# Optimization experiments

Measured on AMD Instinct MI355X. Metric: run time of the kernel, lower is better.

Reference implementation:

```python
import jax, jax.numpy as jnp
import numpy as np

NUM_TOKENS = 32000
DIM = 1024
DEPTH = 4
HEADS = 16
DIM_HEAD = 64
FF_MULT = 4
DH_FF = int(DIM * FF_MULT * 2 / 3)  # 2730
B, N = 2, 2048
ROPE_THETA = 10000.0


def setup_inputs() -> dict:
    key = jax.random.key(0)
    ks = jax.random.split(key, 8)
    s = 0.02
    return {
        "tokens": jax.random.randint(ks[0], (B, N), 0, NUM_TOKENS),
        "token_emb": jax.random.normal(ks[1], (NUM_TOKENS, DIM)) * s,
        "attn_norm_w": jnp.ones((DEPTH, DIM)),
        "wqkv": jax.random.normal(ks[2], (DEPTH, DIM, 3 * HEADS * DIM_HEAD)) * s,
        "wo": jax.random.normal(ks[3], (DEPTH, HEADS * DIM_HEAD, DIM)) * s,
        "ff_norm_w": jnp.ones((DEPTH, DIM)),
        "ff_w1": jax.random.normal(ks[4], (DEPTH, DIM, 2 * DH_FF)) * s,
        "ff_b1": jnp.zeros((DEPTH, 2 * DH_FF)),
        "ff_w2": jax.random.normal(ks[5], (DEPTH, DH_FF, DIM)) * s,
        "ff_b2": jnp.zeros((DEPTH, DIM)),
        "final_norm_w": jnp.ones((DIM,)),
        "logits_w": jax.random.normal(ks[6], (DIM, NUM_TOKENS)) * s,
        "logits_b": jnp.zeros((NUM_TOKENS,)),
    }


def rmsnorm(x, w):
    eps = jnp.finfo(x.dtype).eps  # torch RMSNorm default eps
    var = jnp.mean(jnp.square(x), axis=-1, keepdims=True)
    return x * jax.lax.rsqrt(var + eps) * w


def rotate_half(x):
    x1, x2 = jnp.split(x, 2, axis=-1)
    return jnp.concatenate((-x2, x1), axis=-1)


def apply_rope(pos, t):
    return t * jnp.cos(pos) + rotate_half(t) * jnp.sin(pos)


def reference(tokens, token_emb, attn_norm_w, wqkv, wo, ff_norm_w,
              ff_w1, ff_b1, ff_w2, ff_b2, final_norm_w, logits_w, logits_b):
    b, n = tokens.shape
    x = token_emb[tokens]  # [b, n, dim]

    # rotary embedding table [n, dim_head]
    inv_freq = ROPE_THETA ** (-(jnp.arange(0, DIM_HEAD, 2, dtype=jnp.float32) / DIM_HEAD))
    freqs = jnp.arange(n, dtype=jnp.float32)[:, None] * inv_freq[None, :]
    pos = jnp.concatenate((freqs, freqs), axis=-1)

    scale = DIM_HEAD ** -0.5
    causal = jnp.triu(jnp.ones((n, n), dtype=bool), 1)

    for l in range(DEPTH):
        # --- attention ---
        h = rmsnorm(x, attn_norm_w[l])
        qkv = jnp.einsum('bnd,de->bne', h, wqkv[l])
        qkv = qkv.reshape(b, n, 3, HEADS, DIM_HEAD)
        qkv = jnp.transpose(qkv, (2, 0, 3, 1, 4))  # [3, b, h, n, d]
        q, k, v = qkv[0], qkv[1], qkv[2]
        q = apply_rope(pos, q)
        k = apply_rope(pos, k)
        q = q * scale
        sim = jnp.einsum('bhid,bhjd->bhij', q, k)
        sim = jnp.where(causal, -jnp.finfo(sim.dtype).max, sim)
        attn = jax.nn.softmax(sim, axis=-1)
        out = jnp.einsum('bhij,bhjd->bhid', attn, v)
        out = jnp.transpose(out, (0, 2, 1, 3)).reshape(b, n, HEADS * DIM_HEAD)
        x = jnp.einsum('bne,ed->bnd', out, wo[l]) + x

        # --- GEGLU feedforward ---
        h = rmsnorm(x, ff_norm_w[l])
        u = jnp.einsum('bnd,de->bne', h, ff_w1[l]) + ff_b1[l]
        u1, gate = jnp.split(u, 2, axis=-1)
        g = jax.nn.gelu(gate, approximate=False) * u1
        x = jnp.einsum('bne,ed->bnd', g, ff_w2[l]) + ff_b2[l] + x

    embed = rmsnorm(x, final_norm_w)
    logits = jnp.einsum('bnd,dv->bnv', embed, logits_w) + logits_b
    return logits
```

## Files before the change

### kernel.cpp

```cpp
#include <hip/hip_runtime.h>
#include <math.h>
#include <stdint.h>


using short8v = __attribute__((ext_vector_type(8))) short;
using f32x4   = __attribute__((ext_vector_type(4))) float;

__device__ __forceinline__ float b2f(short s) {
    union { unsigned u; float f; } v; v.u = ((unsigned)(unsigned short)s) << 16; return v.f;
}
__device__ __forceinline__ short f2b(float f) {
    union { float f; unsigned u; } v; v.f = f;
    unsigned r = v.u + 0x7FFFu + ((v.u >> 16) & 1u);
    return (short)(r >> 16);
}

__device__ __forceinline__ void mfma_n(f32x4& d, short8v a, short8v b) {
    asm("v_mfma_f32_16x16x32_bf16 %0, %1, %2, %0" : "+v"(d) : "v"(a), "v"(b));
}
__device__ __forceinline__ void mfma_f(f32x4& d, short8v a, short8v b) {
    asm("s_nop 1\n\tv_mfma_f32_16x16x32_bf16 %0, %1, %2, %0" : "+v"(d) : "v"(a), "v"(b));
}
#define MFMA_FENCE() do { __builtin_amdgcn_sched_barrier(0); \
    asm volatile("s_nop 7\n\ts_nop 7"); \
    __builtin_amdgcn_sched_barrier(0); } while (0)

__device__ __forceinline__ void gload16(const void* g, void* l) {
    __builtin_amdgcn_global_load_lds(
        (const __attribute__((address_space(1))) unsigned int*)(uintptr_t)g,
        (__attribute__((address_space(3))) unsigned int*)(uintptr_t)l,
        16, 0, 0);
}

#define BARX() do { asm volatile("" ::: "memory"); \
    __builtin_amdgcn_s_barrier(); asm volatile("" ::: "memory"); } while (0)
#define VMN(n) asm volatile("s_waitcnt vmcnt(" #n ")" ::: "memory")
#define LGKM0() do { asm volatile("s_waitcnt lgkmcnt(0)" ::: "memory"); \
    __builtin_amdgcn_sched_barrier(0); } while (0)

__global__ void rope_table_k(float* __restrict__ ct, float* __restrict__ st) {
    int i = blockIdx.x * 256 + threadIdx.x;
    int n = i >> 5, j = i & 31;
    float freq = expf(-(float)j * (9.210340371976184f / 32.f));
    float a = (float)n * freq;
    ct[i] = cosf(a);
    st[i] = sinf(a);
}

__global__ void embed_k(const int* __restrict__ tok, const float* __restrict__ emb,
                        float* __restrict__ x) {
    int row = blockIdx.x;
    int tk = tok[row];
    const float4* src = (const float4*)(emb + (size_t)tk * 1024);
    float4* dst = (float4*)(x + (size_t)row * 1024);
    dst[threadIdx.x] = src[threadIdx.x];
}

__global__ void wconv_k(const float* __restrict__ W, short* __restrict__ T,
                        int K, int N, int Kpad,
                        size_t w_lstride, size_t t_lstride) {
    W += blockIdx.z * w_lstride;
    T += blockIdx.z * t_lstride;
    int n0 = blockIdx.x * 32, k0 = blockIdx.y * 32;
    __shared__ float tile[32][33];
    int t = threadIdx.x;
    int kk = t >> 3, ns = (t & 7) * 4;
    float4 v = make_float4(0.f, 0.f, 0.f, 0.f);
    int gk = k0 + kk;
    if (gk < K) {
        if (n0 + ns + 3 < N) {
            v = *(const float4*)(W + (size_t)gk * N + n0 + ns);
        } else {
            float tmp[4] = {0.f, 0.f, 0.f, 0.f};
            #pragma unroll
            for (int j = 0; j < 4; ++j)
                if (n0 + ns + j < N) tmp[j] = W[(size_t)gk * N + n0 + ns + j];
            v = make_float4(tmp[0], tmp[1], tmp[2], tmp[3]);
        }
    }
    tile[kk][ns + 0] = v.x; tile[kk][ns + 1] = v.y;
    tile[kk][ns + 2] = v.z; tile[kk][ns + 3] = v.w;
    __syncthreads();
    int nn = t >> 3, ks = (t & 7) * 4;
    short o[4];
    #pragma unroll
    for (int j = 0; j < 4; ++j) o[j] = f2b(tile[ks + j][nn]);
    *(int2*)(T + (size_t)(n0 + nn) * Kpad + k0 + ks) = *(int2*)o;
}

__global__ void rmsnorm_k(const float* __restrict__ x, const float* __restrict__ wt,
                          short* __restrict__ out) {
    int row = blockIdx.x;
    int t = threadIdx.x;
    const float* xr = x + (size_t)row * 1024;
    float4 v = ((const float4*)xr)[t];
    float ss = v.x * v.x + v.y * v.y + v.z * v.z + v.w * v.w;
    #pragma unroll
    for (int off = 32; off > 0; off >>= 1) ss += __shfl_down(ss, off, 64);
    __shared__ float red[4];
    if ((t & 63) == 0) red[t >> 6] = ss;
    __syncthreads();
    float tot = red[0] + red[1] + red[2] + red[3];
    float inv = rsqrtf(tot * (1.f / 1024.f) + 1.1920929e-7f);
    float4 wv = ((const float4*)wt)[t];
    int2 pk;
    pk.x = (int)(unsigned short)f2b(v.x * inv * wv.x) |
           ((int)(unsigned short)f2b(v.y * inv * wv.y) << 16);
    pk.y = (int)(unsigned short)f2b(v.z * inv * wv.z) |
           ((int)(unsigned short)f2b(v.w * inv * wv.w) << 16);
    *(int2*)(out + (size_t)row * 1024 + t * 4) = pk;
}

__global__ void rope_apply_k(short* __restrict__ qkv, const float* __restrict__ ct,
                             const float* __restrict__ st) {
    int gidx = blockIdx.x * 256 + threadIdx.x;
    int j  = gidx & 31;
    int r  = (gidx >> 5) & 4095;
    int hk = gidx >> 17;
    int qk = hk >> 4, h = hk & 15;
    int n = r & 2047;
    size_t base = (size_t)r * 3072 + (size_t)qk * 1024 + h * 64 + j;
    float a  = b2f(qkv[base]);
    float bv = b2f(qkv[base + 32]);
    float cc = ct[n * 32 + j], sv = st[n * 32 + j];
    float na = a * cc - bv * sv;
    float nb = bv * cc + a * sv;
    if (qk == 0) { na *= 0.125f; nb *= 0.125f; }
    qkv[base]      = f2b(na);
    qkv[base + 32] = f2b(nb);
}

__global__ void vt_k(const short* __restrict__ qkv, short* __restrict__ vt) {
    int id = blockIdx.x * 256 + threadIdx.x;
    int dt = id & 7, nt = (id >> 3) & 255, bh = id >> 11;
    int b = bh >> 4, h = bh & 15;
    short s[8][8];
    #pragma unroll
    for (int r = 0; r < 8; ++r)
        *(int4*)s[r] = *(const int4*)(qkv + (size_t)(b * 2048 + nt * 8 + r) * 3072
                                      + 2048 + h * 64 + dt * 8);
    #pragma unroll
    for (int cc = 0; cc < 8; ++cc) {
        short o4[8];
        #pragma unroll
        for (int r = 0; r < 8; ++r) o4[r] = s[r][cc];
        *(int4*)(vt + (size_t)(bh * 64 + dt * 8 + cc) * 2048 + nt * 8) = *(int4*)o4;
    }
}

__global__ void geglu_k(const short* __restrict__ u, short* __restrict__ gbuf) {
    int r = blockIdx.x;
    int c = blockIdx.y * 256 + threadIdx.x;
    if (c >= 2752) return;
    float v = 0.f;
    if (c < 2730) {
        float u1 = b2f(u[(size_t)r * 5460 + c]);
        float gt = b2f(u[(size_t)r * 5460 + 2730 + c]);
        v = 0.5f * gt * (1.f + erff(gt * 0.7071067811865475f)) * u1;
    }
    gbuf[(size_t)r * 2752 + c] = f2b(v);
}

template <bool BIAS, bool RES, bool OUTBF16>
__global__ __launch_bounds__(256, 2) void gemm2(
    const short* __restrict__ A, const short* __restrict__ Bt,
    const float* __restrict__ bias, const float* __restrict__ res,
    void* __restrict__ outp, int N, int lda, int ldb, int ksteps) {
    __shared__ __align__(16) short As[128 * 32];
    __shared__ __align__(16) short Bs[128 * 32];
    const int t = threadIdx.x;
    const int lane = t & 63;
    const int w = t >> 6, wm = w >> 1, wn = w & 1;
    const int c = lane & 15, g = lane >> 4;

    const int nwg = (int)gridDim.x;
    const int cpx = nwg >> 3;
    const int wg = ((int)blockIdx.x & 7) * cpx + ((int)blockIdx.x >> 3);
    const int m0 = (wg & 31) << 7;
    const int n0 = (wg >> 5) << 7;

    const int srow = w * 32 + (lane >> 2);
    const int sseg = (lane & 3) * 8;
    const short* ga0 = A  + (size_t)(m0 + srow) * lda + sseg;
    const short* ga1 = A  + (size_t)(m0 + srow + 16) * lda + sseg;
    const short* gb0 = Bt + (size_t)(n0 + srow) * ldb + sseg;
    const short* gb1 = Bt + (size_t)(n0 + srow + 16) * ldb + sseg;
    short* la0 = &As[(w * 2 + 0) * 512];
    short* la1 = &As[(w * 2 + 1) * 512];
    short* lb0 = &Bs[(w * 2 + 0) * 512];
    short* lb1 = &Bs[(w * 2 + 1) * 512];

    f32x4 acc[4][4] = {};

    for (int kt = 0; kt < ksteps; ++kt) {
        const int k0 = kt << 5;
        __syncthreads();
        gload16(ga0 + k0, la0);
        gload16(ga1 + k0, la1);
        gload16(gb0 + k0, lb0);
        gload16(gb1 + k0, lb1);
        __syncthreads();
        short8v af[4], bf[4];
        #pragma unroll
        for (int mi = 0; mi < 4; ++mi)
            af[mi] = *(const short8v*)&As[(wm * 64 + mi * 16 + c) * 32 + g * 8];
        #pragma unroll
        for (int ni = 0; ni < 4; ++ni)
            bf[ni] = *(const short8v*)&Bs[(wn * 64 + ni * 16 + c) * 32 + g * 8];
        #pragma unroll
        for (int mi = 0; mi < 4; ++mi)
            #pragma unroll
            for (int ni = 0; ni < 4; ++ni)
                mfma_n(acc[mi][ni], af[mi], bf[ni]);
    }
    MFMA_FENCE();
    #pragma unroll
    for (int mi = 0; mi < 4; ++mi) {
        #pragma unroll
        for (int ni = 0; ni < 4; ++ni) {
            int col = n0 + wn * 64 + ni * 16 + c;
            if (col < N) {
                float bv = BIAS ? bias[col] : 0.f;
                #pragma unroll
                for (int i = 0; i < 4; ++i) {
                    int row = m0 + wm * 64 + mi * 16 + g * 4 + i;
                    size_t off = (size_t)row * N + col;
                    float v = acc[mi][ni][i] + bv;
                    if (RES) v += res[off];
                    if (OUTBF16) ((short*)outp)[off] = f2b(v);
                    else         ((float*)outp)[off] = v;
                }
            }
        }
    }
}

template <bool BIAS, bool RES, bool OUTBF16>
__global__ __launch_bounds__(512, 1) void gemm3(
    const short* __restrict__ A, const short* __restrict__ Bt,
    const float* __restrict__ bias, const float* __restrict__ res,
    void* __restrict__ outp, int N, int lda, int ldb, int nrowsB, int KT) {
    __shared__ __align__(16) short L[49152];
    const int t = threadIdx.x;
    const int lane = t & 63;
    const int w = t >> 6;
    const int wm = w >> 2, wn = w & 3;
    const int c = lane & 15, g = lane >> 4;

    const int nwg = (int)gridDim.x, cpx = nwg >> 3;
    const int wg = ((int)blockIdx.x & 7) * cpx + ((int)blockIdx.x >> 3);
    const int m0 = (wg & 31) << 7;
    const int n0 = (wg >> 5) << 8;

    const int rS = t >> 3, sS = t & 7;
    const int sSw = (sS ^ (rS & 7)) << 3;
    size_t aoffh[2], broff[2][2];
    #pragma unroll
    for (int h = 0; h < 2; ++h)
        aoffh[h] = (size_t)(m0 + h * 64 + rS) * lda + sSw;
    #pragma unroll
    for (int h = 0; h < 2; ++h)
        #pragma unroll
        for (int i = 0; i < 2; ++i) {
            int brow = n0 + h * 128 + rS + i * 64;
            if (brow > nrowsB - 1) brow = nrowsB - 1;
            broff[h][i] = (size_t)brow * ldb + sSw;
        }
    short* ldsA[2][2];
    short* ldsB[2][2];
    #pragma unroll
    for (int p = 0; p < 2; ++p)
        #pragma unroll
        for (int h = 0; h < 2; ++h) {
            ldsA[p][h] = &L[(p * 2 + h) * 4096 + w * 512];
            ldsB[p][h] = &L[16384 + (p * 2 + h) * 8192 + w * 512];
        }

    const int cb0 = ((g * 8) ^ ((c & 7) * 8));
    const int vbA0 = wm * 4096 + c * 64 + cb0;
    const int vbA1 = vbA0 ^ 32;
    const int vbB0 = 16384 + (wn >> 1) * 8192 + (wn & 1) * 4096 + c * 64 + cb0;
    const int vbB1 = vbB0 ^ 32;

    #define STA3(p, h, kt) gload16(A + aoffh[h] + (kt) * 64, ldsA[p][h])
    #define STB3(p, h, kt) do { \
        gload16(Bt + broff[h][0] + (kt) * 64, ldsB[p][h]); \
        gload16(Bt + broff[h][1] + (kt) * 64, ldsB[p][h] + 4096); } while (0)
    #define LDA3(p, mi, ks) (*(const short8v*)&L[(p) * 8192 + (mi) * 1024 + ((ks) ? vbA1 : vbA0)])
    #define LDB3(p, ni, ks) (*(const short8v*)&L[(p) * 16384 + (ni) * 1024 + ((ks) ? vbB1 : vbB0)])
    #define MFMA8(MLO, NLO, BV) do { \
        _Pragma("unroll") for (int ks_ = 0; ks_ < 2; ++ks_) \
        _Pragma("unroll") for (int mi_ = 0; mi_ < 2; ++mi_) \
        _Pragma("unroll") for (int ni_ = 0; ni_ < 2; ++ni_) \
            mfma_n(acc[(MLO) + mi_][(NLO) + ni_], av[(MLO) + mi_][ks_], BV[(NLO) + ni_][ks_]); \
        } while (0)

    f32x4 acc[4][4] = {};
    short8v av[4][2], bc[4][2], bn[4][2];

    STB3(0, 1, 0); STB3(0, 0, 0); STA3(0, 0, 0); STA3(0, 1, 0);
    STB3(1, 1, 1); STB3(1, 0, 1); STA3(1, 0, 1); STA3(1, 1, 1);
    VMN(6);
    BARX();
    #pragma unroll
    for (int ni = 0; ni < 4; ++ni)
        #pragma unroll
        for (int ks = 0; ks < 2; ++ks)
            bc[ni][ks] = LDB3(0, ni, ks);
    LGKM0();
    BARX();
    asm volatile("s_nop 7\n\ts_nop 7");

    for (int KB = 0; KB < KT; KB += 2) {
        const bool st1 = (KB + 2 < KT);
        const bool st2 = (KB + 3 < KT);
        #pragma unroll
        for (int mi = 0; mi < 2; ++mi)
            #pragma unroll
            for (int ks = 0; ks < 2; ++ks) av[mi][ks] = LDA3(0, mi, ks);
        if (st1) STB3(0, 1, KB + 2);
        BARX();
        __builtin_amdgcn_s_setprio(1); MFMA8(0, 0, bc); __builtin_amdgcn_s_setprio(0);
        BARX();
        #pragma unroll
        for (int mi = 2; mi < 4; ++mi)
            #pragma unroll
            for (int ks = 0; ks < 2; ++ks) av[mi][ks] = LDA3(0, mi, ks);
        if (st1) { STB3(0, 0, KB + 2); VMN(6); } else { VMN(2); }
        BARX();
        __builtin_amdgcn_s_setprio(1); MFMA8(2, 0, bc); __builtin_amdgcn_s_setprio(0);
        BARX();
        #pragma unroll
        for (int ni = 0; ni < 2; ++ni)
            #pragma unroll
            for (int ks = 0; ks < 2; ++ks) bn[ni][ks] = LDB3(1, ni, ks);
        if (st1) STA3(0, 0, KB + 2);
        BARX();
        __builtin_amdgcn_s_setprio(1); MFMA8(0, 2, bc); __builtin_amdgcn_s_setprio(0);
        BARX();
        #pragma unroll
        for (int ni = 2; ni < 4; ++ni)
            #pragma unroll
            for (int ks = 0; ks < 2; ++ks) bn[ni][ks] = LDB3(1, ni, ks);
        if (st1) { STA3(0, 1, KB + 2); VMN(6); } else { VMN(0); }
        BARX();
        __builtin_amdgcn_s_setprio(1); MFMA8(2, 2, bc); __builtin_amdgcn_s_setprio(0);
        BARX();
        #pragma unroll
        for (int mi = 0; mi < 2; ++mi)
            #pragma unroll
            for (int ks = 0; ks < 2; ++ks) av[mi][ks] = LDA3(1, mi, ks);
        if (st2) STB3(1, 1, KB + 3);
        BARX();
        __builtin_amdgcn_s_setprio(1); MFMA8(0, 0, bn); __builtin_amdgcn_s_setprio(0);
        BARX();
        #pragma unroll
        for (int mi = 2; mi < 4; ++mi)
            #pragma unroll
            for (int ks = 0; ks < 2; ++ks) av[mi][ks] = LDA3(1, mi, ks);
        if (st2) STB3(1, 0, KB + 3);
        if (st1) VMN(6);
        BARX();
        __builtin_amdgcn_s_setprio(1); MFMA8(2, 0, bn); __builtin_amdgcn_s_setprio(0);
        BARX();
        if (st1) {
            #pragma unroll
            for (int ni = 0; ni < 2; ++ni)
                #pragma unroll
                for (int ks = 0; ks < 2; ++ks) bc[ni][ks] = LDB3(0, ni, ks);
        }
        if (st2) STA3(1, 0, KB + 3);
        BARX();
        __builtin_amdgcn_s_setprio(1); MFMA8(0, 2, bn); __builtin_amdgcn_s_setprio(0);
        BARX();
        if (st1) {
            #pragma unroll
            for (int ni = 2; ni < 4; ++ni)
                #pragma unroll
                for (int ks = 0; ks < 2; ++ks) bc[ni][ks] = LDB3(0, ni, ks);
        }
        if (st2) STA3(1, 1, KB + 3);
        if (st1) VMN(6);
        BARX();
        __builtin_amdgcn_s_setprio(1); MFMA8(2, 2, bn); __builtin_amdgcn_s_setprio(0);
        BARX();
    }

    MFMA_FENCE();
    #pragma unroll
    for (int mi = 0; mi < 4; ++mi) {
        #pragma unroll
        for (int ni = 0; ni < 4; ++ni) {
            int col = n0 + wn * 64 + ni * 16 + c;
            if (col < N) {
                float bv = BIAS ? bias[col] : 0.f;
                #pragma unroll
                for (int i = 0; i < 4; ++i) {
                    int row = m0 + wm * 64 + mi * 16 + g * 4 + i;
                    size_t off = (size_t)row * N + col;
                    float v = acc[mi][ni][i] + bv;
                    if (RES) v += res[off];
                    if (OUTBF16) ((short*)outp)[off] = f2b(v);
                    else         ((float*)outp)[off] = v;
                }
            }
        }
    }
    #undef STA3
    #undef STB3
    #undef LDA3
    #undef LDB3
    #undef MFMA8
}

__global__ __launch_bounds__(256, 2) void attn_fwd(
    const short* __restrict__ qkv, const short* __restrict__ vt,
    short* __restrict__ o) {
    const int qt = blockIdx.x, bh = blockIdx.y;
    const int b = bh >> 4, h = bh & 15;
    const int t = threadIdx.x, lane = t & 63, w = t >> 6;
    const int c = lane & 15, g = lane >> 4;
    __shared__ __align__(16) short Ks[128 * 72];
    __shared__ __align__(16) short Vs[64 * 136];
    __shared__ __align__(16) short Ps[128 * 136];

    #pragma unroll
    for (int i = 0; i < 4; ++i) {
        int idx = t + i * 256, r = idx >> 3, seg = idx & 7;
        *(int4*)&Ps[r * 136 + seg * 8] =
            *(const int4*)(qkv + (size_t)(b * 2048 + qt * 128 + r) * 3072 + h * 64 + seg * 8);
    }
    __syncthreads();
    short8v qf[2][2];
    #pragma unroll
    for (int mi = 0; mi < 2; ++mi)
        #pragma unroll
        for (int kk = 0; kk < 2; ++kk)
            qf[mi][kk] = *(const short8v*)&Ps[(w * 32 + mi * 16 + c) * 136 + kk * 32 + g * 8];

    f32x4 oacc[2][4] = {};
    float mrow[2][4], lrow[2][4];
    #pragma unroll
    for (int mi = 0; mi < 2; ++mi)
        #pragma unroll
        for (int i = 0; i < 4; ++i) { mrow[mi][i] = -3.0e38f; lrow[mi][i] = 0.f; }

    for (int jt = 0; jt <= qt; ++jt) {
        __syncthreads();
        #pragma unroll
        for (int i = 0; i < 4; ++i) {
            int idx = t + i * 256, r = idx >> 3, seg = idx & 7;
            *(int4*)&Ks[r * 72 + seg * 8] =
                *(const int4*)(qkv + (size_t)(b * 2048 + jt * 128 + r) * 3072
                               + 1024 + h * 64 + seg * 8);
        }
        #pragma unroll
        for (int i = 0; i < 4; ++i) {
            int idx = t + i * 256, d = idx >> 4, seg = idx & 15;
            *(int4*)&Vs[d * 136 + seg * 8] =
                *(const int4*)(vt + (size_t)(bh * 64 + d) * 2048 + jt * 128 + seg * 8);
        }
        __syncthreads();
        f32x4 sacc[2][8] = {};
        #pragma unroll
        for (int kk = 0; kk < 2; ++kk) {
            short8v kf[8];
            #pragma unroll
            for (int ni = 0; ni < 8; ++ni)
                kf[ni] = *(const short8v*)&Ks[(ni * 16 + c) * 72 + kk * 32 + g * 8];
            #pragma unroll
            for (int mi = 0; mi < 2; ++mi)
                #pragma unroll
                for (int ni = 0; ni < 8; ++ni) {
                    if (kk == 0) mfma_f(sacc[mi][ni], qf[mi][kk], kf[ni]);
                    else         mfma_n(sacc[mi][ni], qf[mi][kk], kf[ni]);
                }
        }
        MFMA_FENCE();
        if (jt == qt) {
            #pragma unroll
            for (int mi = 0; mi < 2; ++mi)
                #pragma unroll
                for (int ni = 0; ni < 8; ++ni)
                    #pragma unroll
                    for (int i = 0; i < 4; ++i) {
                        int qrow = w * 32 + mi * 16 + g * 4 + i;
                        int kcol = ni * 16 + c;
                        if (kcol > qrow) sacc[mi][ni][i] = -3.0e38f;
                    }
        }
        #pragma unroll
        for (int mi = 0; mi < 2; ++mi) {
            #pragma unroll
            for (int i = 0; i < 4; ++i) {
                float mx = sacc[mi][0][i];
                #pragma unroll
                for (int ni = 1; ni < 8; ++ni) mx = fmaxf(mx, sacc[mi][ni][i]);
                #pragma unroll
                for (int off = 1; off < 16; off <<= 1) mx = fmaxf(mx, __shfl_xor(mx, off, 64));
                float mnew = fmaxf(mrow[mi][i], mx);
                float alpha = __expf(mrow[mi][i] - mnew);
                mrow[mi][i] = mnew;
                float ls = 0.f;
                #pragma unroll
                for (int ni = 0; ni < 8; ++ni) {
                    float p = __expf(sacc[mi][ni][i] - mnew);
                    sacc[mi][ni][i] = p;
                    ls += p;
                }
                #pragma unroll
                for (int off = 1; off < 16; off <<= 1) ls += __shfl_xor(ls, off, 64);
                lrow[mi][i] = lrow[mi][i] * alpha + ls;
                #pragma unroll
                for (int df = 0; df < 4; ++df) oacc[mi][df][i] *= alpha;
            }
        }
        #pragma unroll
        for (int mi = 0; mi < 2; ++mi)
            #pragma unroll
            for (int ni = 0; ni < 8; ++ni)
                #pragma unroll
                for (int i = 0; i < 4; ++i)
                    Ps[(w * 32 + mi * 16 + g * 4 + i) * 136 + ni * 16 + c] =
                        f2b(sacc[mi][ni][i]);
        #pragma unroll
        for (int kk = 0; kk < 4; ++kk) {
            short8v pf[2], vf[4];
            #pragma unroll
            for (int mi = 0; mi < 2; ++mi)
                pf[mi] = *(const short8v*)&Ps[(w * 32 + mi * 16 + c) * 136 + kk * 32 + g * 8];
            #pragma unroll
            for (int df = 0; df < 4; ++df)
                vf[df] = *(const short8v*)&Vs[(df * 16 + c) * 136 + kk * 32 + g * 8];
            #pragma unroll
            for (int mi = 0; mi < 2; ++mi)
                #pragma unroll
                for (int df = 0; df < 4; ++df) {
                    if (kk == 0) mfma_f(oacc[mi][df], pf[mi], vf[df]);
                    else         mfma_n(oacc[mi][df], pf[mi], vf[df]);
                }
        }
    }
    MFMA_FENCE();
    #pragma unroll
    for (int mi = 0; mi < 2; ++mi)
        #pragma unroll
        for (int df = 0; df < 4; ++df)
            #pragma unroll
            for (int i = 0; i < 4; ++i) {
                int qrow = qt * 128 + w * 32 + mi * 16 + g * 4 + i;
                float v = oacc[mi][df][i] / lrow[mi][i];
                o[(size_t)(b * 2048 + qrow) * 1024 + h * 64 + df * 16 + c] = f2b(v);
            }
}

extern "C" void kernel_launch(void* const* d_in, const int* in_sizes, int n_in,
                              void* d_out, int out_size, void* d_ws, size_t ws_size,
                              hipStream_t stream) {
    (void)in_sizes; (void)n_in; (void)out_size; (void)ws_size;
    const int*   tokens = (const int*)d_in[0];
    const float* temb   = (const float*)d_in[1];
    const float* anw    = (const float*)d_in[2];
    const float* wqkv   = (const float*)d_in[3];
    const float* wo     = (const float*)d_in[4];
    const float* fnw    = (const float*)d_in[5];
    const float* fw1    = (const float*)d_in[6];
    const float* fb1    = (const float*)d_in[7];
    const float* fw2    = (const float*)d_in[8];
    const float* fb2    = (const float*)d_in[9];
    const float* finw   = (const float*)d_in[10];
    const float* lw     = (const float*)d_in[11];
    const float* lb     = (const float*)d_in[12];

    char* ws = (char*)d_ws;
    float* x    = (float*)(ws + 0);
    short* hb   = (short*)(ws + 16777216);
    short* qkv  = (short*)(ws + 25165824);
    short* ao   = (short*)(ws + 50331648);
    short* ub   = (short*)(ws + 58720256);
    short* gb   = (short*)(ws + 103448576);
    short* vtb  = (short*)(ws + 125992960);
    float* ct   = (float*)(ws + 134381568);
    float* st   = (float*)(ws + 134643712);
    short* qkvT = (short*)(ws + 134905856);
    short* woT  = (short*)(ws + 160071680);
    short* fw1T = (short*)(ws + 168460288);
    short* fw2T = (short*)(ws + 213549056);
    short* logT = (short*)(ws + 236093440);

    rope_table_k<<<256, 256, 0, stream>>>(ct, st);
    embed_k<<<4096, 256, 0, stream>>>(tokens, temb, x);

    wconv_k<<<dim3(96, 32, 4), 256, 0, stream>>>(
        wqkv, qkvT, 1024, 3072, 1024, (size_t)1024 * 3072, (size_t)3072 * 1024);
    wconv_k<<<dim3(32, 32, 4), 256, 0, stream>>>(
        wo, woT, 1024, 1024, 1024, (size_t)1024 * 1024, (size_t)1024 * 1024);
    wconv_k<<<dim3(172, 32, 4), 256, 0, stream>>>(
        fw1, fw1T, 1024, 5460, 1024, (size_t)1024 * 5460, (size_t)5504 * 1024);
    wconv_k<<<dim3(32, 86, 4), 256, 0, stream>>>(
        fw2, fw2T, 2730, 1024, 2752, (size_t)2730 * 1024, (size_t)1024 * 2752);
    wconv_k<<<dim3(1000, 32, 1), 256, 0, stream>>>(
        lw, logT, 1024, 32000, 1024, 0, 0);

    for (int l = 0; l < 4; ++l) {
        rmsnorm_k<<<4096, 256, 0, stream>>>(x, anw + l * 1024, hb);
        gemm3<false, false, true><<<32 * 12, 512, 0, stream>>>(
            hb, qkvT + (size_t)l * 3072 * 1024, nullptr, nullptr, qkv,
            3072, 1024, 1024, 3072, 16);
        rope_apply_k<<<16384, 256, 0, stream>>>(qkv, ct, st);
        vt_k<<<256, 256, 0, stream>>>(qkv, vtb);
        attn_fwd<<<dim3(16, 32), 256, 0, stream>>>(qkv, vtb, ao);
        gemm2<false, true, false><<<32 * 8, 256, 0, stream>>>(
            ao, woT + (size_t)l * 1024 * 1024, nullptr, x, x, 1024, 1024, 1024, 32);
        rmsnorm_k<<<4096, 256, 0, stream>>>(x, fnw + l * 1024, hb);
        gemm3<true, false, true><<<32 * 22, 512, 0, stream>>>(
            hb, fw1T + (size_t)l * 5504 * 1024, fb1 + l * 5460, nullptr, ub,
            5460, 1024, 1024, 5504, 16);
        geglu_k<<<dim3(4096, 11), 256, 0, stream>>>(ub, gb);
        gemm2<true, true, false><<<32 * 8, 256, 0, stream>>>(
            gb, fw2T + (size_t)l * 1024 * 2752, fb2 + l * 1024, x, x, 1024, 2752, 2752, 86);
    }
    rmsnorm_k<<<4096, 256, 0, stream>>>(x, finw, hb);
    gemm3<true, false, false><<<32 * 125, 512, 0, stream>>>(
        hb, logT, lb, nullptr, d_out, 32000, 1024, 1024, 32000, 16);
}
```

Baseline: 2.059 ms.

## Fuse RoPE into QKV GEMM epilogue and add larger-tile logits GEMM

Removes the separate rope_apply_k pass by applying rotary embedding and the q scale inside the QKV GEMM epilogue, where each wave's 64-column tile holds both halves of a head. Also adds a new gemm4 kernel with 256x256 tiles, two workgroups per CU and a different LDS staging layout, and uses it for the final 32000-wide logits projection. The fusion saves one read-modify-write pass over the qkv buffer per layer. The new logits kernel aims to raise operand reuse on the largest GEMM, at the cost of more accumulator registers and LDS per workgroup.

```diff
diff --git a/kernel.cpp b/kernel.cpp
--- a/kernel.cpp
+++ b/kernel.cpp
@@ -111,25 +111,6 @@
     *(int2*)(out + (size_t)row * 1024 + t * 4) = pk;
 }
 
-__global__ void rope_apply_k(short* __restrict__ qkv, const float* __restrict__ ct,
-                             const float* __restrict__ st) {
-    int gidx = blockIdx.x * 256 + threadIdx.x;
-    int j  = gidx & 31;
-    int r  = (gidx >> 5) & 4095;
-    int hk = gidx >> 17;
-    int qk = hk >> 4, h = hk & 15;
-    int n = r & 2047;
-    size_t base = (size_t)r * 3072 + (size_t)qk * 1024 + h * 64 + j;
-    float a  = b2f(qkv[base]);
-    float bv = b2f(qkv[base + 32]);
-    float cc = ct[n * 32 + j], sv = st[n * 32 + j];
-    float na = a * cc - bv * sv;
-    float nb = bv * cc + a * sv;
-    if (qk == 0) { na *= 0.125f; nb *= 0.125f; }
-    qkv[base]      = f2b(na);
-    qkv[base + 32] = f2b(nb);
-}
-
 __global__ void vt_k(const short* __restrict__ qkv, short* __restrict__ vt) {
     int id = blockIdx.x * 256 + threadIdx.x;
     int dt = id & 7, nt = (id >> 3) & 255, bh = id >> 11;
@@ -235,11 +216,12 @@
     }
 }
 
-template <bool BIAS, bool RES, bool OUTBF16>
+template <bool BIAS, bool RES, bool OUTBF16, bool ROPE>
 __global__ __launch_bounds__(512, 1) void gemm3(
     const short* __restrict__ A, const short* __restrict__ Bt,
     const float* __restrict__ bias, const float* __restrict__ res,
-    void* __restrict__ outp, int N, int lda, int ldb, int nrowsB, int KT) {
+    void* __restrict__ outp, int N, int lda, int ldb, int nrowsB, int KT,
+    const float* __restrict__ ct, const float* __restrict__ st) {
     __shared__ __align__(16) short L[49152];
     const int t = threadIdx.x;
     const int lane = t & 63;
@@ -387,6 +369,44 @@
     }
 
     MFMA_FENCE();
+
+    if (ROPE) {
+        const int colbase = n0 + wn * 64;
+        const int sec = colbase >> 10;
+        if (sec < 2) {
+            const float sc = (sec == 0) ? 0.125f : 1.0f;
+            #pragma unroll
+            for (int mi = 0; mi < 4; ++mi)
+                #pragma unroll
+                for (int ni = 0; ni < 2; ++ni) {
+                    const int col = colbase + ni * 16 + c;
+                    const int jj = ni * 16 + c;
+                    #pragma unroll
+                    for (int i = 0; i < 4; ++i) {
+                        int row = m0 + wm * 64 + mi * 16 + g * 4 + i;
+                        int n = row & 2047;
+                        float cv = ct[n * 32 + jj], sv = st[n * 32 + jj];
+                        float a = acc[mi][ni][i], b = acc[mi][ni + 2][i];
+                        ((short*)outp)[(size_t)row * N + col]      = f2b((a * cv - b * sv) * sc);
+                        ((short*)outp)[(size_t)row * N + col + 32] = f2b((b * cv + a * sv) * sc);
+                    }
+                }
+        } else {
+            #pragma unroll
+            for (int mi = 0; mi < 4; ++mi)
+                #pragma unroll
+                for (int ni = 0; ni < 4; ++ni) {
+                    int col = colbase + ni * 16 + c;
+                    #pragma unroll
+                    for (int i = 0; i < 4; ++i) {
+                        int row = m0 + wm * 64 + mi * 16 + g * 4 + i;
+                        ((short*)outp)[(size_t)row * N + col] = f2b(acc[mi][ni][i]);
+                    }
+                }
+        }
+        return;
+    }
+
     #pragma unroll
     for (int mi = 0; mi < 4; ++mi) {
         #pragma unroll
@@ -411,6 +431,115 @@
     #undef LDA3
     #undef LDB3
     #undef MFMA8
+}
+
+template <bool BIAS, bool RES, bool OUTBF16>
+__global__ __launch_bounds__(512, 2) void gemm4(
+    const short* __restrict__ A, const short* __restrict__ Bt,
+    const float* __restrict__ bias, const float* __restrict__ res,
+    void* __restrict__ outp, int N, int lda, int ldb, int nrowsB, int KT) {
+    __shared__ __align__(16) short L[65536];
+    const int t = threadIdx.x;
+    const int lane = t & 63;
+    const int w = t >> 6;
+    const int wm = w >> 2, wn = w & 3;
+    const int c = lane & 15, g = lane >> 4;
+
+    const int nwg = (int)gridDim.x, cpx = nwg >> 3;
+    const int wg = ((int)blockIdx.x & 7) * cpx + ((int)blockIdx.x >> 3);
+    const int m0 = (wg & 15) << 8;
+    const int n0 = (wg >> 4) << 8;
+
+    const int sub0 = t & 63;
+    const int seg0 = sub0 >> 4, r0 = sub0 & 15;
+    const int slab0 = t >> 6, slab1 = slab0 + 8;
+    const size_t aoff0 = (size_t)(m0 + slab0 * 16 + r0) * lda + seg0 * 8;
+    const size_t aoff1 = (size_t)(m0 + slab1 * 16 + r0) * lda + seg0 * 8;
+    int br0 = n0 + slab0 * 16 + r0; if (br0 > nrowsB - 1) br0 = nrowsB - 1;
+    int br1 = n0 + slab1 * 16 + r0; if (br1 > nrowsB - 1) br1 = nrowsB - 1;
+    const size_t boff0 = (size_t)br0 * ldb + seg0 * 8;
+    const size_t boff1 = (size_t)br1 * ldb + seg0 * 8;
+
+    char* Lb = (char*)L;
+    const int rb = g * 256 + c * 16;
+
+    #define STA4(p, kh, kt) do { \
+        gload16(A + aoff0 + (kt) * 64 + (kh) * 32, Lb + ((p)*2+(kh))*16384 + w*1024); \
+        gload16(A + aoff1 + (kt) * 64 + (kh) * 32, Lb + ((p)*2+(kh))*16384 + 8192 + w*1024); } while (0)
+    #define STB4(p, kh, kt) do { \
+        gload16(Bt + boff0 + (kt) * 64 + (kh) * 32, Lb + 65536 + ((p)*2+(kh))*16384 + w*1024); \
+        gload16(Bt + boff1 + (kt) * 64 + (kh) * 32, Lb + 65536 + ((p)*2+(kh))*16384 + 8192 + w*1024); } while (0)
+    #define LDA4(p, ks, mi) (*(const short8v*)(Lb + ((p)*2+(ks))*16384 + (wm*8+(mi))*1024 + rb))
+    #define LDB4(p, ks, ni) (*(const short8v*)(Lb + 65536 + ((p)*2+(ks))*16384 + (wn*4+(ni))*1024 + rb))
+    #define MFMAQ(MB) do { \
+        _Pragma("unroll") for (int mi_ = 0; mi_ < 4; ++mi_) \
+        _Pragma("unroll") for (int ni_ = 0; ni_ < 4; ++ni_) \
+            mfma_n(acc[(MB) + mi_][ni_], av[mi_], bv[ni_]); } while (0)
+
+    f32x4 acc[8][4] = {};
+    short8v av[4], bv[4];
+
+    STA4(0, 0, 0); STB4(0, 0, 0); STA4(0, 1, 0); STB4(0, 1, 0);
+    VMN(4);
+    BARX();
+    asm volatile("s_nop 7\n\ts_nop 7");
+
+    #define TILE4(p, pn, tc, stg2) do { \
+        _Pragma("unroll") for (int mi = 0; mi < 4; ++mi) av[mi] = LDA4(p, 0, mi); \
+        _Pragma("unroll") for (int ni = 0; ni < 4; ++ni) bv[ni] = LDB4(p, 0, ni); \
+        if (stg2) STA4(pn, 0, (tc) + 1); \
+        BARX(); \
+        __builtin_amdgcn_s_setprio(1); MFMAQ(0); __builtin_amdgcn_s_setprio(0); \
+        BARX(); \
+        _Pragma("unroll") for (int mi = 0; mi < 4; ++mi) av[mi] = LDA4(p, 0, mi + 4); \
+        if (stg2) { STB4(pn, 0, (tc) + 1); VMN(4); } else { VMN(0); } \
+        BARX(); \
+        __builtin_amdgcn_s_setprio(1); MFMAQ(4); __builtin_amdgcn_s_setprio(0); \
+        BARX(); \
+        _Pragma("unroll") for (int mi = 0; mi < 4; ++mi) av[mi] = LDA4(p, 1, mi); \
+        _Pragma("unroll") for (int ni = 0; ni < 4; ++ni) bv[ni] = LDB4(p, 1, ni); \
+        if (stg2) STA4(pn, 1, (tc) + 1); \
+        BARX(); \
+        __builtin_amdgcn_s_setprio(1); MFMAQ(0); __builtin_amdgcn_s_setprio(0); \
+        BARX(); \
+        _Pragma("unroll") for (int mi = 0; mi < 4; ++mi) av[mi] = LDA4(p, 1, mi + 4); \
+        if (stg2) { STB4(pn, 1, (tc) + 1); VMN(4); } \
+        BARX(); \
+        __builtin_amdgcn_s_setprio(1); MFMAQ(4); __builtin_amdgcn_s_setprio(0); \
+        BARX(); \
+    } while (0)
+
+    for (int kt = 0; kt < KT; kt += 2) {
+        TILE4(0, 1, kt, true);
+        TILE4(1, 0, kt + 1, (kt + 2 < KT));
+    }
+    #undef TILE4
+
+    MFMA_FENCE();
+    #pragma unroll
+    for (int mi = 0; mi < 8; ++mi) {
+        #pragma unroll
+        for (int ni = 0; ni < 4; ++ni) {
+            int col = n0 + wn * 64 + ni * 16 + c;
+            if (col < N) {
+                float bvv = BIAS ? bias[col] : 0.f;
+                #pragma unroll
+                for (int i = 0; i < 4; ++i) {
+                    int row = m0 + wm * 128 + mi * 16 + g * 4 + i;
+                    size_t off = (size_t)row * N + col;
+                    float v = acc[mi][ni][i] + bvv;
+                    if (RES) v += res[off];
+                    if (OUTBF16) ((short*)outp)[off] = f2b(v);
+                    else         ((float*)outp)[off] = v;
+                }
+            }
+        }
+    }
+    #undef STA4
+    #undef STB4
+    #undef LDA4
+    #undef LDB4
+    #undef MFMAQ
 }
 
 __global__ __launch_bounds__(256, 2) void attn_fwd(
@@ -604,23 +733,22 @@
 
     for (int l = 0; l < 4; ++l) {
         rmsnorm_k<<<4096, 256, 0, stream>>>(x, anw + l * 1024, hb);
-        gemm3<false, false, true><<<32 * 12, 512, 0, stream>>>(
+        gemm3<false, false, true, true><<<32 * 12, 512, 0, stream>>>(
             hb, qkvT + (size_t)l * 3072 * 1024, nullptr, nullptr, qkv,
-            3072, 1024, 1024, 3072, 16);
-        rope_apply_k<<<16384, 256, 0, stream>>>(qkv, ct, st);
+            3072, 1024, 1024, 3072, 16, ct, st);
         vt_k<<<256, 256, 0, stream>>>(qkv, vtb);
         attn_fwd<<<dim3(16, 32), 256, 0, stream>>>(qkv, vtb, ao);
         gemm2<false, true, false><<<32 * 8, 256, 0, stream>>>(
             ao, woT + (size_t)l * 1024 * 1024, nullptr, x, x, 1024, 1024, 1024, 32);
         rmsnorm_k<<<4096, 256, 0, stream>>>(x, fnw + l * 1024, hb);
-        gemm3<true, false, true><<<32 * 22, 512, 0, stream>>>(
+        gemm3<true, false, true, false><<<32 * 22, 512, 0, stream>>>(
             hb, fw1T + (size_t)l * 5504 * 1024, fb1 + l * 5460, nullptr, ub,
-            5460, 1024, 1024, 5504, 16);
+            5460, 1024, 1024, 5504, 16, nullptr, nullptr);
         geglu_k<<<dim3(4096, 11), 256, 0, stream>>>(ub, gb);
         gemm2<true, true, false><<<32 * 8, 256, 0, stream>>>(
             gb, fw2T + (size_t)l * 1024 * 2752, fb2 + l * 1024, x, x, 1024, 2752, 2752, 86);
     }
     rmsnorm_k<<<4096, 256, 0, stream>>>(x, finw, hb);
-    gemm3<true, false, false><<<32 * 125, 512, 0, stream>>>(
+    gemm4<true, false, false><<<2000, 512, 0, stream>>>(
         hb, logT, lb, nullptr, d_out, 32000, 1024, 1024, 32000, 16);
 }
```

New measurement: 2.017 ms. 1.02x faster.
